# Performance work log

Measured on AMD Instinct MI355X. Metric: run time of the kernel, lower is better.

The kernel has to match this reference:

```python
import jax, jax.numpy as jnp
import numpy as np

B, T, D, H = 64, 512, 256, 1024
INIT_S = 0.005


def setup_inputs() -> dict:
    key = jax.random.key(0)
    ks = jax.random.split(key, 8)
    gate_bias = float(np.log(INIT_S / (1.0 - INIT_S)))
    # Linear weights in torch layout [out, in]; y = x @ W.T + b.
    # Gate weights (Ws, Us) are zero-init in the module; we use small random
    # values so the gate path actually exercises the math.
    return {
        "x": jax.random.normal(ks[0], (B, T, D), dtype=jnp.float32),
        "Wx_w": jax.random.normal(ks[1], (H, D), dtype=jnp.float32) / np.sqrt(D),
        "Wx_b": jnp.zeros((H,), dtype=jnp.float32),
        "Wh_w": jax.random.normal(ks[2], (H, H), dtype=jnp.float32) / np.sqrt(H),
        "Ws_w": jax.random.normal(ks[3], (1, D), dtype=jnp.float32) * 0.01,
        "Ws_b": jnp.full((1,), gate_bias, dtype=jnp.float32),
        "Us_w": jax.random.normal(ks[4], (1, H), dtype=jnp.float32) * 0.01,
        "out_w": jax.random.normal(ks[5], (1, H), dtype=jnp.float32) / np.sqrt(H),
        "out_b": jnp.zeros((1,), dtype=jnp.float32),
    }


def reference(x, Wx_w, Wx_b, Wh_w, Ws_w, Ws_b, Us_w, out_w, out_b):
    # SharedGateRNN.forward_with_intermediates (ln=False, gate_rescale=None)
    wh_diag = jnp.diagonal(Wh_w)        # [H]
    us_vec = Us_w.reshape(-1)           # [H]

    def step(h_prev, x_t):
        # x_t: [B, D], h_prev: [B, H]
        a_s = x_t @ Ws_w.T + Ws_b + h_prev @ Us_w.T     # [B, 1]
        s = jax.nn.sigmoid(a_s)                          # [B, 1] scalar gate
        pre = x_t @ Wx_w.T + Wx_b + h_prev @ Wh_w.T      # [B, H]
        h_tilde = jnp.tanh(pre)
        h = (1.0 - s) * h_prev + s * h_tilde             # broadcast gate over H
        y = h @ out_w.T + out_b                          # [B, 1]
        gate_s = jnp.broadcast_to(s, h.shape)
        leak = 1.0 - gate_s
        tanh_prime = 1.0 - h_tilde ** 2
        s_prime = s * (1.0 - s)                          # [B, 1]
        rdiag = (h_tilde - h_prev) * (s_prime * us_vec) + s * tanh_prime * wh_diag
        return h, (y, h, gate_s, leak, rdiag)

    h0 = jnp.zeros((x.shape[0], H), dtype=x.dtype)
    x_t_first = jnp.transpose(x, (1, 0, 2))              # [T, B, D]
    _, (ys, hs, gates, leaks, rdiags) = jax.lax.scan(step, h0, x_t_first)

    swap = lambda a: jnp.transpose(a, (1, 0, 2))         # [T,B,*] -> [B,T,*]
    return (swap(ys), swap(hs), swap(gates), swap(leaks), swap(rdiags))
```

## Files before the change

kernel.cpp:

```cpp
#include <hip/hip_runtime.h>

#define NT 512
#define ND 256
#define NH 1024
#define NB 64

typedef float f32x4 __attribute__((ext_vector_type(4)));
typedef short bf16x8 __attribute__((ext_vector_type(8)));

__device__ __forceinline__ unsigned short f2bf(float f) {
  unsigned u = __builtin_bit_cast(unsigned, f);
  u += 0x7fffu + ((u >> 16) & 1u);
  return (unsigned short)(u >> 16);
}
__device__ __forceinline__ float bflo(unsigned u) {
  return __builtin_bit_cast(float, u << 16);
}
__device__ __forceinline__ float bfhi(unsigned u) {
  return __builtin_bit_cast(float, u & 0xffff0000u);
}
__device__ __forceinline__ bf16x8 pack8(float4 a, float4 b) {
  bf16x8 r;
  r[0] = (short)f2bf(a.x); r[1] = (short)f2bf(a.y);
  r[2] = (short)f2bf(a.z); r[3] = (short)f2bf(a.w);
  r[4] = (short)f2bf(b.x); r[5] = (short)f2bf(b.y);
  r[6] = (short)f2bf(b.z); r[7] = (short)f2bf(b.w);
  return r;
}

__global__ void __launch_bounds__(256, 1)
rnn_step_kernel(const float* __restrict__ x,
                const float* __restrict__ Wx_w,
                const float* __restrict__ Wx_b,
                const float* __restrict__ Wh_w,
                const float* __restrict__ Ws_w,
                const float* __restrict__ Ws_b,
                const float* __restrict__ Us_w,
                float* __restrict__ out,
                unsigned short* __restrict__ hbuf,
                unsigned int* __restrict__ flags)
{
  const int tid = (int)threadIdx.x;
  const int w   = tid >> 6;
  const int l   = tid & 63;
  const int bm  = l & 15;
  const int lg  = l >> 4;
  const int sl  = (int)blockIdx.x & 63;
  const int bg  = (int)blockIdx.x >> 6;
  const int r_base = sl * 16;
  const int b_base = bg * 16;
  const int bo = tid & 15;
  const int ro = tid >> 4;
  const int rg = r_base + ro;
  const int b_glob = b_base + bo;

  __shared__ unsigned short h_sh[16][1024];
  __shared__ unsigned short x_sh[16][256];
  __shared__ unsigned short us_sh[1024];
  __shared__ unsigned short ws_sh[256];
  __shared__ float cpart[4][4][64];
  __shared__ float gpart[4][16];

  {
    const float4 uv = *(const float4*)(Us_w + tid*4);
    us_sh[tid*4+0] = f2bf(uv.x); us_sh[tid*4+1] = f2bf(uv.y);
    us_sh[tid*4+2] = f2bf(uv.z); us_sh[tid*4+3] = f2bf(uv.w);
    if (tid < 64) {
      const float4 wv = *(const float4*)(Ws_w + tid*4);
      ws_sh[tid*4+0] = f2bf(wv.x); ws_sh[tid*4+1] = f2bf(wv.y);
      ws_sh[tid*4+2] = f2bf(wv.z); ws_sh[tid*4+3] = f2bf(wv.w);
    }
  }

  bf16x8 whf[8];
  bf16x8 wxf[2];
  {
    const int ar = r_base + bm;
    #pragma unroll
    for (int m = 0; m < 8; ++m) {
      const int k0 = w*256 + m*32 + lg*8;
      const float4 f0 = *(const float4*)(Wh_w + (size_t)ar*NH + k0);
      const float4 f1 = *(const float4*)(Wh_w + (size_t)ar*NH + k0 + 4);
      whf[m] = pack8(f0, f1);
    }
    #pragma unroll
    for (int m = 0; m < 2; ++m) {
      const int k0 = w*64 + m*32 + lg*8;
      const float4 f0 = *(const float4*)(Wx_w + (size_t)ar*ND + k0);
      const float4 f1 = *(const float4*)(Wx_w + (size_t)ar*ND + k0 + 4);
      wxf[m] = pack8(f0, f1);
    }
  }
  const float wxb_r = Wx_b[rg];
  const float whd_r = Wh_w[(size_t)rg*NH + rg];
  const float usr_r = Us_w[rg];
  const float wsb   = Ws_b[0];

  float* const hs_o = out + (size_t)NB*NT;
  float* const g_o  = hs_o + (size_t)NB*NT*NH;
  float* const l_o  = g_o  + (size_t)NB*NT*NH;
  float* const rd_o = l_o  + (size_t)NB*NT*NH;

  float myh = 0.f;

  for (int t = 0; t < NT; ++t) {
    #pragma unroll
    for (int it = 0; it < 4; ++it) {
      const int f4 = tid + it*256;
      const int b  = f4 >> 6;
      const int d4 = f4 & 63;
      const float4 xv = *(const float4*)(x + ((size_t)(b_base+b)*NT + t)*ND + d4*4);
      const int c = (d4 >> 1) ^ (b & 7);
      const unsigned p0 = (unsigned)f2bf(xv.x) | ((unsigned)f2bf(xv.y) << 16);
      const unsigned p1 = (unsigned)f2bf(xv.z) | ((unsigned)f2bf(xv.w) << 16);
      *(uint2*)&x_sh[b][c*8 + (d4 & 1)*4] = make_uint2(p0, p1);
    }
    __syncthreads();

    f32x4 acc = {0.f, 0.f, 0.f, 0.f};
    float ga = 0.f;
    #pragma unroll
    for (int m = 0; m < 2; ++m) {
      const int c0 = (w*8 + m*4 + lg) ^ (bm & 7);
      const uint4 bxu = *(const uint4*)&x_sh[bm][c0*8];
      acc = __builtin_amdgcn_mfma_f32_16x16x32_bf16(
              wxf[m], __builtin_bit_cast(bf16x8, bxu), acc, 0, 0, 0);
      const int ku = w*64 + m*32 + lg*8;
      const uint4 uu = *(const uint4*)&ws_sh[ku];
      ga += bflo(uu.x)*bflo(bxu.x) + bfhi(uu.x)*bfhi(bxu.x);
      ga += bflo(uu.y)*bflo(bxu.y) + bfhi(uu.y)*bfhi(bxu.y);
      ga += bflo(uu.z)*bflo(bxu.z) + bfhi(uu.z)*bfhi(bxu.z);
      ga += bflo(uu.w)*bflo(bxu.w) + bfhi(uu.w)*bfhi(bxu.w);
    }

    if (t > 0) {
      if (w == 0) {
        const unsigned int* fp = flags + ((size_t)bg*NT + (t-1))*64 + l;
        while (true) {
          unsigned int v;
          asm volatile("global_load_dword %0, %1, off sc0 sc1\n\t"
                       "s_waitcnt vmcnt(0)"
                       : "=v"(v) : "v"(fp) : "memory");
          if (__all((int)(v != 0u))) break;
          __builtin_amdgcn_s_sleep(1);
        }
      }
      __syncthreads();
      {
        const unsigned short* src = hbuf + ((size_t)((t-1)&1)*NB + b_base)*NH;
        uint4 hv[8];
        #pragma unroll
        for (int it = 0; it < 8; ++it) {
          const int f4 = tid + it*256;
          const unsigned short* a = src + (size_t)(f4 >> 7)*NH + (f4 & 127)*8;
          asm volatile("global_load_dwordx4 %0, %1, off sc0 sc1"
                       : "=v"(hv[it]) : "v"(a) : "memory");
        }
        asm volatile("s_waitcnt vmcnt(0)" ::: "memory");
        __builtin_amdgcn_sched_barrier(0);
        #pragma unroll
        for (int it = 0; it < 8; ++it) {
          const int f4 = tid + it*256;
          const int b = f4 >> 7, c = f4 & 127;
          *(uint4*)&h_sh[b][(c ^ (b & 7))*8] = hv[it];
        }
      }
      __syncthreads();

      #pragma unroll
      for (int m = 0; m < 8; ++m) {
        const int c0 = (w*32 + m*4 + lg) ^ (bm & 7);
        const uint4 bhu = *(const uint4*)&h_sh[bm][c0*8];
        acc = __builtin_amdgcn_mfma_f32_16x16x32_bf16(
                whf[m], __builtin_bit_cast(bf16x8, bhu), acc, 0, 0, 0);
        const int ku = w*256 + m*32 + lg*8;
        const uint4 uu = *(const uint4*)&us_sh[ku];
        ga += bflo(uu.x)*bflo(bhu.x) + bfhi(uu.x)*bfhi(bhu.x);
        ga += bflo(uu.y)*bflo(bhu.y) + bfhi(uu.y)*bfhi(bhu.y);
        ga += bflo(uu.z)*bflo(bhu.z) + bfhi(uu.z)*bfhi(bhu.z);
        ga += bflo(uu.w)*bflo(bhu.w) + bfhi(uu.w)*bfhi(bhu.w);
      }
    }

    ga += __shfl_xor(ga, 16, 64);
    ga += __shfl_xor(ga, 32, 64);
    if (l < 16) gpart[w][l] = ga;
    cpart[w][0][l] = acc[0];
    cpart[w][1][l] = acc[1];
    cpart[w][2][l] = acc[2];
    cpart[w][3][l] = acc[3];
    __syncthreads();

    const float gsum = gpart[0][bo] + gpart[1][bo] + gpart[2][bo] + gpart[3][bo];
    const int ci = ro & 3, cl = (ro >> 2)*16 + bo;
    const float pre0 = cpart[0][ci][cl] + cpart[1][ci][cl] +
                       cpart[2][ci][cl] + cpart[3][ci][cl];
    const float sg   = 1.f / (1.f + expf(-(gsum + wsb)));
    const float pre  = pre0 + wxb_r;
    const float htld = tanhf(pre);
    const float hp   = myh;
    const float h    = (1.f - sg)*hp + sg*htld;
    myh = h;
    {
      const unsigned hb = (unsigned)f2bf(h);
      unsigned short* hp2 = hbuf + ((size_t)(t & 1)*NB + b_glob)*NH + rg;
      asm volatile("global_store_short %0, %1, off sc0 sc1"
                   :: "v"(hp2), "v"(hb) : "memory");
    }
    asm volatile("s_waitcnt vmcnt(0)" ::: "memory");
    __syncthreads();
    if (tid == 0) {
      unsigned int one = 1u;
      unsigned int* fp = flags + ((size_t)bg*NT + t)*64 + sl;
      asm volatile("global_store_dword %0, %1, off sc0 sc1"
                   :: "v"(fp), "v"(one) : "memory");
    }

    {
      const size_t obase = ((size_t)b_glob*NT + t)*NH + rg;
      const float sp = sg * (1.f - sg);
      __builtin_nontemporal_store(h, &hs_o[obase]);
      __builtin_nontemporal_store(sg, &g_o[obase]);
      __builtin_nontemporal_store(1.f - sg, &l_o[obase]);
      __builtin_nontemporal_store((htld - hp)*(sp*usr_r) + sg*(1.f - htld*htld)*whd_r,
                                  &rd_o[obase]);
    }
  }
}

__global__ void yfinish_kernel(const float* __restrict__ hs,
                               const float* __restrict__ out_w,
                               const float* __restrict__ out_b,
                               float* __restrict__ ys)
{
  const int row  = (int)blockIdx.x*4 + ((int)threadIdx.x >> 6);
  const int lane = (int)threadIdx.x & 63;
  const float4* hp = (const float4*)(hs + (size_t)row*NH);
  const float4* wp = (const float4*)out_w;
  float s = 0.f;
  #pragma unroll
  for (int i = 0; i < 4; ++i) {
    const float4 h4 = hp[i*64 + lane];
    const float4 w4 = wp[i*64 + lane];
    s += h4.x*w4.x + h4.y*w4.y + h4.z*w4.z + h4.w*w4.w;
  }
  #pragma unroll
  for (int off = 32; off > 0; off >>= 1) s += __shfl_xor(s, off, 64);
  if (lane == 0) ys[row] = s + out_b[0];
}

extern "C" void kernel_launch(void* const* d_in, const int* in_sizes, int n_in,
                              void* d_out, int out_size, void* d_ws, size_t ws_size,
                              hipStream_t stream)
{
  (void)in_sizes; (void)n_in; (void)out_size; (void)ws_size;
  const float* x     = (const float*)d_in[0];
  const float* Wx_w  = (const float*)d_in[1];
  const float* Wx_b  = (const float*)d_in[2];
  const float* Wh_w  = (const float*)d_in[3];
  const float* Ws_w  = (const float*)d_in[4];
  const float* Ws_b  = (const float*)d_in[5];
  const float* Us_w  = (const float*)d_in[6];
  const float* out_w = (const float*)d_in[7];
  const float* out_b = (const float*)d_in[8];
  float* out = (float*)d_out;

  char* ws = (char*)d_ws;
  unsigned short* hbuf = (unsigned short*)ws;
  unsigned int* flags  = (unsigned int*)(ws + 262144);

  hipMemsetAsync(flags, 0, (size_t)4*NT*64*sizeof(unsigned int), stream);
  rnn_step_kernel<<<dim3(256), dim3(256), 0, stream>>>(
      x, Wx_w, Wx_b, Wh_w, Ws_w, Ws_b, Us_w, out, hbuf, flags);
  yfinish_kernel<<<dim3((NB*NT)/4), dim3(256), 0, stream>>>(
      out + (size_t)NB*NT, out_w, out_b, out);
}
```

Measured before the change: 2.065 ms.

## Load x and h operands directly into MFMA registers, dropping LDS staging and barriers

```diff
diff --git a/kernel.cpp b/kernel.cpp
--- a/kernel.cpp
+++ b/kernel.cpp
@@ -49,31 +49,24 @@
   const int bg  = (int)blockIdx.x >> 6;
   const int r_base = sl * 16;
   const int b_base = bg * 16;
-  const int bo = tid & 15;
-  const int ro = tid >> 4;
+  const int ro = tid & 15;
+  const int bo = tid >> 4;
   const int rg = r_base + ro;
   const int b_glob = b_base + bo;
 
-  __shared__ unsigned short h_sh[16][1024];
-  __shared__ unsigned short x_sh[16][256];
   __shared__ unsigned short us_sh[1024];
-  __shared__ unsigned short ws_sh[256];
-  __shared__ float cpart[4][4][64];
+  __shared__ float cpart[4][4][72];
   __shared__ float gpart[4][16];
 
   {
     const float4 uv = *(const float4*)(Us_w + tid*4);
     us_sh[tid*4+0] = f2bf(uv.x); us_sh[tid*4+1] = f2bf(uv.y);
     us_sh[tid*4+2] = f2bf(uv.z); us_sh[tid*4+3] = f2bf(uv.w);
-    if (tid < 64) {
-      const float4 wv = *(const float4*)(Ws_w + tid*4);
-      ws_sh[tid*4+0] = f2bf(wv.x); ws_sh[tid*4+1] = f2bf(wv.y);
-      ws_sh[tid*4+2] = f2bf(wv.z); ws_sh[tid*4+3] = f2bf(wv.w);
-    }
   }
 
   bf16x8 whf[8];
   bf16x8 wxf[2];
+  float4 wsf[4];
   {
     const int ar = r_base + bm;
     #pragma unroll
@@ -89,6 +82,8 @@
       const float4 f0 = *(const float4*)(Wx_w + (size_t)ar*ND + k0);
       const float4 f1 = *(const float4*)(Wx_w + (size_t)ar*ND + k0 + 4);
       wxf[m] = pack8(f0, f1);
+      wsf[m*2]   = *(const float4*)(Ws_w + k0);
+      wsf[m*2+1] = *(const float4*)(Ws_w + k0 + 4);
     }
   }
   const float wxb_r = Wx_b[rg];
@@ -101,40 +96,28 @@
   float* const l_o  = g_o  + (size_t)NB*NT*NH;
   float* const rd_o = l_o  + (size_t)NB*NT*NH;
 
+  __syncthreads();
+
   float myh = 0.f;
 
   for (int t = 0; t < NT; ++t) {
-    #pragma unroll
-    for (int it = 0; it < 4; ++it) {
-      const int f4 = tid + it*256;
-      const int b  = f4 >> 6;
-      const int d4 = f4 & 63;
-      const float4 xv = *(const float4*)(x + ((size_t)(b_base+b)*NT + t)*ND + d4*4);
-      const int c = (d4 >> 1) ^ (b & 7);
-      const unsigned p0 = (unsigned)f2bf(xv.x) | ((unsigned)f2bf(xv.y) << 16);
-      const unsigned p1 = (unsigned)f2bf(xv.z) | ((unsigned)f2bf(xv.w) << 16);
-      *(uint2*)&x_sh[b][c*8 + (d4 & 1)*4] = make_uint2(p0, p1);
-    }
-    __syncthreads();
-
     f32x4 acc = {0.f, 0.f, 0.f, 0.f};
     float ga = 0.f;
-    #pragma unroll
-    for (int m = 0; m < 2; ++m) {
-      const int c0 = (w*8 + m*4 + lg) ^ (bm & 7);
-      const uint4 bxu = *(const uint4*)&x_sh[bm][c0*8];
-      acc = __builtin_amdgcn_mfma_f32_16x16x32_bf16(
-              wxf[m], __builtin_bit_cast(bf16x8, bxu), acc, 0, 0, 0);
-      const int ku = w*64 + m*32 + lg*8;
-      const uint4 uu = *(const uint4*)&ws_sh[ku];
-      ga += bflo(uu.x)*bflo(bxu.x) + bfhi(uu.x)*bfhi(bxu.x);
-      ga += bflo(uu.y)*bflo(bxu.y) + bfhi(uu.y)*bfhi(bxu.y);
-      ga += bflo(uu.z)*bflo(bxu.z) + bfhi(uu.z)*bfhi(bxu.z);
-      ga += bflo(uu.w)*bflo(bxu.w) + bfhi(uu.w)*bfhi(bxu.w);
+    {
+      const float* xrow = x + ((size_t)(b_base+bm)*NT + t)*ND + w*64 + lg*8;
+      #pragma unroll
+      for (int m = 0; m < 2; ++m) {
+        const float4 f0 = *(const float4*)(xrow + m*32);
+        const float4 f1 = *(const float4*)(xrow + m*32 + 4);
+        acc = __builtin_amdgcn_mfma_f32_16x16x32_bf16(
+                wxf[m], pack8(f0, f1), acc, 0, 0, 0);
+        ga += wsf[m*2].x*f0.x + wsf[m*2].y*f0.y + wsf[m*2].z*f0.z + wsf[m*2].w*f0.w
+            + wsf[m*2+1].x*f1.x + wsf[m*2+1].y*f1.y + wsf[m*2+1].z*f1.z + wsf[m*2+1].w*f1.w;
+      }
     }
 
     if (t > 0) {
-      if (w == 0) {
+      {
         const unsigned int* fp = flags + ((size_t)bg*NT + (t-1))*64 + l;
         while (true) {
           unsigned int v;
@@ -145,40 +128,24 @@
           __builtin_amdgcn_s_sleep(1);
         }
       }
-      __syncthreads();
-      {
-        const unsigned short* src = hbuf + ((size_t)((t-1)&1)*NB + b_base)*NH;
-        uint4 hv[8];
-        #pragma unroll
-        for (int it = 0; it < 8; ++it) {
-          const int f4 = tid + it*256;
-          const unsigned short* a = src + (size_t)(f4 >> 7)*NH + (f4 & 127)*8;
-          asm volatile("global_load_dwordx4 %0, %1, off sc0 sc1"
-                       : "=v"(hv[it]) : "v"(a) : "memory");
-        }
-        asm volatile("s_waitcnt vmcnt(0)" ::: "memory");
-        __builtin_amdgcn_sched_barrier(0);
-        #pragma unroll
-        for (int it = 0; it < 8; ++it) {
-          const int f4 = tid + it*256;
-          const int b = f4 >> 7, c = f4 & 127;
-          *(uint4*)&h_sh[b][(c ^ (b & 7))*8] = hv[it];
-        }
-      }
-      __syncthreads();
-
+      const unsigned short* hrow =
+          hbuf + ((size_t)((t-1)&1)*NB + b_base + bm)*NH + w*256 + lg*8;
+      uint4 hv[8];
+      #pragma unroll
+      for (int m = 0; m < 8; ++m)
+        asm volatile("global_load_dwordx4 %0, %1, off sc0 sc1"
+                     : "=v"(hv[m]) : "v"(hrow + m*32) : "memory");
+      asm volatile("s_waitcnt vmcnt(0)" ::: "memory");
+      __builtin_amdgcn_sched_barrier(0);
       #pragma unroll
       for (int m = 0; m < 8; ++m) {
-        const int c0 = (w*32 + m*4 + lg) ^ (bm & 7);
-        const uint4 bhu = *(const uint4*)&h_sh[bm][c0*8];
         acc = __builtin_amdgcn_mfma_f32_16x16x32_bf16(
-                whf[m], __builtin_bit_cast(bf16x8, bhu), acc, 0, 0, 0);
-        const int ku = w*256 + m*32 + lg*8;
-        const uint4 uu = *(const uint4*)&us_sh[ku];
-        ga += bflo(uu.x)*bflo(bhu.x) + bfhi(uu.x)*bfhi(bhu.x);
-        ga += bflo(uu.y)*bflo(bhu.y) + bfhi(uu.y)*bfhi(bhu.y);
-        ga += bflo(uu.z)*bflo(bhu.z) + bfhi(uu.z)*bfhi(bhu.z);
-        ga += bflo(uu.w)*bflo(bhu.w) + bfhi(uu.w)*bfhi(bhu.w);
+                whf[m], __builtin_bit_cast(bf16x8, hv[m]), acc, 0, 0, 0);
+        const uint4 uu = *(const uint4*)&us_sh[w*256 + m*32 + lg*8];
+        ga += bflo(uu.x)*bflo(hv[m].x) + bfhi(uu.x)*bfhi(hv[m].x)
+            + bflo(uu.y)*bflo(hv[m].y) + bfhi(uu.y)*bfhi(hv[m].y)
+            + bflo(uu.z)*bflo(hv[m].z) + bfhi(uu.z)*bfhi(hv[m].z)
+            + bflo(uu.w)*bflo(hv[m].w) + bfhi(uu.w)*bfhi(hv[m].w);
       }
     }
 
@@ -192,7 +159,7 @@
     __syncthreads();
 
     const float gsum = gpart[0][bo] + gpart[1][bo] + gpart[2][bo] + gpart[3][bo];
-    const int ci = ro & 3, cl = (ro >> 2)*16 + bo;
+    const int ci = ro & 3, cl = ((ro >> 2) << 4) + bo;
     const float pre0 = cpart[0][ci][cl] + cpart[1][ci][cl] +
                        cpart[2][ci][cl] + cpart[3][ci][cl];
     const float sg   = 1.f / (1.f + expf(-(gsum + wsb)));
@@ -203,9 +170,9 @@
     myh = h;
     {
       const unsigned hb = (unsigned)f2bf(h);
-      unsigned short* hp2 = hbuf + ((size_t)(t & 1)*NB + b_glob)*NH + rg;
+      unsigned short* hptr = hbuf + ((size_t)(t & 1)*NB + b_glob)*NH + rg;
       asm volatile("global_store_short %0, %1, off sc0 sc1"
-                   :: "v"(hp2), "v"(hb) : "memory");
+                   :: "v"(hptr), "v"(hb) : "memory");
     }
     asm volatile("s_waitcnt vmcnt(0)" ::: "memory");
     __syncthreads();
```

Result: faster. 1.834 ms (-11.2%).
